# Optimization experiments

Measured on AMD Instinct MI355X. Metric: run time of the kernel, lower is better.

The kernel has to match this reference:

```python
import math
import jax, jax.numpy as jnp
import numpy as np

CT = {"SDD": 1000.0, "SCD": 500.0, "det_interval": 1.0, "num_det": 736}


def ramp_filter_np(ct, scale):
    # Standard equiangular fan-beam ramp filter (utility.ramp_filter):
    #   h[0] = 1/(8*db^2); h[n odd] = -1/(2*(pi*sin(n*db))^2); h[n even!=0] = 0
    db = ct["det_interval"] / ct["SDD"] * scale  # angular detector pitch at this scale
    n_det = int(ct["num_det"] // scale)
    n = np.arange(-(n_det - 1), n_det)  # length K = 2*n_det - 1
    h = np.zeros(n.shape, dtype=np.float32)
    h[n == 0] = 1.0 / (8.0 * db ** 2)
    odd = (n % 2) != 0
    h[odd] = -0.5 / (np.pi * np.sin(n[odd] * db)) ** 2
    return h


def setup_inputs() -> dict:
    key = jax.random.key(0)
    scale = 1
    batch, ch, view, det = 16, 1, 1152, CT["num_det"] // scale
    sinogram = jax.random.normal(key, (batch, ch, view, det), dtype=jnp.float32)
    delta_b = CT["det_interval"] / CT["SDD"]
    # recon_filter = ramp_filter * scale * delta_b, shaped [1,1,1,K] (OIHW)
    filt = ramp_filter_np(CT, scale) * scale * delta_b
    recon_filter = jnp.asarray(filt, dtype=jnp.float32)[None, None, None, :]
    return {"sinogram": sinogram, "recon_filter": recon_filter, "scale": scale}


def reference(sinogram, recon_filter, scale):
    det = sinogram.shape[-1]
    # cosine fan-beam pre-weighting
    s_range = (CT["det_interval"]
               * jnp.linspace((1.0 - det) / 2.0, (det - 1.0) / 2.0, det, dtype=jnp.float32)
               * scale) / CT["SDD"]
    cos_weight = (CT["SCD"] / 10000.0) * jnp.cos(s_range)  # [det]
    x = sinogram * cos_weight[None, None, None, :]
    # 1D ramp-filter convolution along detector axis (F.conv2d with 1xK kernel)
    K = recon_filter.shape[-1]
    pad = K // 2
    out = jax.lax.conv_general_dilated(
        x, recon_filter,
        window_strides=(1, 1),
        padding=[(0, 0), (pad, pad)],
        dimension_numbers=("NCHW", "OIHW", "NCHW"),
    )
    return out
```

## Files before the change

### kernel.cpp

```cpp
#include <hip/hip_runtime.h>

typedef unsigned short ushort_t;
typedef ushort_t u16x8 __attribute__((ext_vector_type(8)));
typedef __bf16 bf16x8 __attribute__((ext_vector_type(8)));
typedef float f32x4 __attribute__((ext_vector_type(4)));

#define DET 736
#define NPAD 768
#define NKB 23
#define NBY 12

__device__ __forceinline__ ushort_t f2bf(float f) {
    unsigned u = __builtin_bit_cast(unsigned, f);
    u += 0x7FFFu + ((u >> 16) & 1u);
    return (ushort_t)(u >> 16);
}

__global__ void cast_swz_a(const float* __restrict__ in, ushort_t* __restrict__ out) {
    int t = blockIdx.x * 256 + threadIdx.x;
    int l  = t & 63;
    int fi = t >> 6;
    int kb = fi % NKB;
    int rs = fi / NKB;
    int row = rs * 16 + (l & 15);
    int k0  = kb * 32 + (l >> 4) * 8;
    const float* p = in + row * DET + k0;
    float4 a = *(const float4*)p;
    float4 b = *(const float4*)(p + 4);
    u16x8 o;
    o[0] = f2bf(a.x); o[1] = f2bf(a.y); o[2] = f2bf(a.z); o[3] = f2bf(a.w);
    o[4] = f2bf(b.x); o[5] = f2bf(b.y); o[6] = f2bf(b.z); o[7] = f2bf(b.w);
    *(u16x8*)(out + (size_t)t * 8) = o;
}

__global__ void prep_bt_swz(const float* __restrict__ filt, ushort_t* __restrict__ B) {
    int G = blockIdx.x * 256 + threadIdx.x;
    int l  = G & 63;
    int ns = (G >> 6) & 3;
    int kb = (G >> 8) % NKB;
    int by = (G >> 8) / NKB;
    int col = by * 64 + ns * 16 + (l & 15);
    int k0  = kb * 32 + (l >> 4) * 8;
    u16x8 o;
#pragma unroll
    for (int j = 0; j < 8; ++j) {
        int k = k0 + j;
        float w = 0.05f * cosf(((float)k - 367.5f) * 0.001f);
        float v = (col < DET) ? w * filt[k - col + (DET - 1)] : 0.0f;
        o[j] = f2bf(v);
    }
    *(u16x8*)(B + (size_t)G * 8) = o;
}

__global__ __launch_bounds__(256, 3) void gemm_nb(
    const ushort_t* __restrict__ A,
    const ushort_t* __restrict__ B,
    float* __restrict__ C)
{
    __shared__ ushort_t Bs[12 * 256 * 8];

    const int tid  = threadIdx.x;
    const int lane = tid & 63;
    const int w    = tid >> 6;
    const int quad = lane >> 4;
    const int l16  = lane & 15;
    const int bx = blockIdx.x, by = blockIdx.y;

    const ushort_t* pA = A + ((size_t)(bx * 16 + w * 4) * NKB * 64 + lane) * 8;
    const ushort_t* pB = B + (size_t)by * (NKB * 256) * 8;

    f32x4 acc[4][4];
#pragma unroll
    for (int i = 0; i < 4; ++i)
#pragma unroll
        for (int j = 0; j < 4; ++j)
            acc[i][j] = (f32x4){0.f, 0.f, 0.f, 0.f};

#define STAGE(CHUNKS, OFF)                                            \
    for (int c = tid; c < (CHUNKS); c += 256)                         \
        *(u16x8*)(Bs + (size_t)c * 8) = *(const u16x8*)(pB + ((size_t)(OFF) + c) * 8);

#define BODY(KB, KB0)                                                          \
    {                                                                          \
        u16x8 af[4], bf[4];                                                    \
        _Pragma("unroll")                                                      \
        for (int mi = 0; mi < 4; ++mi)                                         \
            af[mi] = *(const u16x8*)(pA + ((size_t)mi * NKB * 64 + (KB) * 64) * 8); \
        _Pragma("unroll")                                                      \
        for (int ni = 0; ni < 4; ++ni)                                         \
            bf[ni] = *(const u16x8*)(Bs + (((KB) - (KB0)) * 256 + ni * 64 + lane) * 8); \
        _Pragma("unroll")                                                      \
        for (int mi = 0; mi < 4; ++mi)                                         \
            _Pragma("unroll")                                                  \
            for (int ni = 0; ni < 4; ++ni)                                     \
                acc[mi][ni] = __builtin_amdgcn_mfma_f32_16x16x32_bf16(         \
                    __builtin_bit_cast(bf16x8, af[mi]),                        \
                    __builtin_bit_cast(bf16x8, bf[ni]),                        \
                    acc[mi][ni], 0, 0, 0);                                     \
    }

    STAGE(12 * 256, 0)
    __syncthreads();
#pragma unroll
    for (int kb = 0; kb < 12; ++kb) BODY(kb, 0)
    __syncthreads();
    STAGE(11 * 256, 12 * 256)
    __syncthreads();
#pragma unroll
    for (int kb = 12; kb < 23; ++kb) BODY(kb, 12)

#pragma unroll
    for (int mi = 0; mi < 4; ++mi) {
#pragma unroll
        for (int ni = 0; ni < 4; ++ni) {
            int colg = by * 64 + ni * 16 + l16;
            if (colg < DET) {
#pragma unroll
                for (int r = 0; r < 4; ++r) {
                    size_t rowg = (size_t)bx * 256 + w * 64 + mi * 16 + quad * 4 + r;
                    C[rowg * DET + colg] = acc[mi][ni][r];
                }
            }
        }
    }
#undef STAGE
#undef BODY
}

extern "C" void kernel_launch(void* const* d_in, const int* in_sizes, int n_in,
                              void* d_out, int out_size, void* d_ws, size_t ws_size,
                              hipStream_t stream) {
    const float* sino = (const float*)d_in[0];
    const float* filt = (const float*)d_in[1];
    int total = in_sizes[0];

    ushort_t* Aswz = (ushort_t*)d_ws;
    ushort_t* Bswz = Aswz + (size_t)total;
    float* out = (float*)d_out;

    cast_swz_a<<<total / 8 / 256, 256, 0, stream>>>(sino, Aswz);
    prep_bt_swz<<<(NBY * NKB * 4 * 64) / 256, 256, 0, stream>>>(filt, Bswz);

    dim3 grid(18432 / 256, NBY);
    gemm_nb<<<grid, 256, 0, stream>>>(Aswz, Bswz, out);
}
```

Before: 144.0 us.

## Fuse fp32-to-bf16 cast of sinogram into GEMM, stage A in LDS

Removes the separate cast/swizzle kernel and its bf16 workspace round-trip. Each GEMM block now loads 32 rows of fp32 sinogram, converts them to bf16 into shared memory, and computes all 736 output columns. Each wave covers three column panels and reads the filter matrix B directly from global memory (L2) rather than staging it in LDS. This saves a kernel launch and the A write/read traffic, but every block re-reads the whole B matrix, the grid becomes a single 1D dimension of 576 blocks, and each block does less A reuse per B load.

```diff
diff --git a/kernel.cpp b/kernel.cpp
--- a/kernel.cpp
+++ b/kernel.cpp
@@ -6,31 +6,13 @@
 typedef float f32x4 __attribute__((ext_vector_type(4)));
 
 #define DET 736
-#define NPAD 768
 #define NKB 23
-#define NBY 12
+#define NPAN 12
 
 __device__ __forceinline__ ushort_t f2bf(float f) {
     unsigned u = __builtin_bit_cast(unsigned, f);
     u += 0x7FFFu + ((u >> 16) & 1u);
     return (ushort_t)(u >> 16);
-}
-
-__global__ void cast_swz_a(const float* __restrict__ in, ushort_t* __restrict__ out) {
-    int t = blockIdx.x * 256 + threadIdx.x;
-    int l  = t & 63;
-    int fi = t >> 6;
-    int kb = fi % NKB;
-    int rs = fi / NKB;
-    int row = rs * 16 + (l & 15);
-    int k0  = kb * 32 + (l >> 4) * 8;
-    const float* p = in + row * DET + k0;
-    float4 a = *(const float4*)p;
-    float4 b = *(const float4*)(p + 4);
-    u16x8 o;
-    o[0] = f2bf(a.x); o[1] = f2bf(a.y); o[2] = f2bf(a.z); o[3] = f2bf(a.w);
-    o[4] = f2bf(b.x); o[5] = f2bf(b.y); o[6] = f2bf(b.z); o[7] = f2bf(b.w);
-    *(u16x8*)(out + (size_t)t * 8) = o;
 }
 
 __global__ void prep_bt_swz(const float* __restrict__ filt, ushort_t* __restrict__ B) {
@@ -52,79 +34,83 @@
     *(u16x8*)(B + (size_t)G * 8) = o;
 }
 
-__global__ __launch_bounds__(256, 3) void gemm_nb(
-    const ushort_t* __restrict__ A,
+__global__ __launch_bounds__(256, 3) void gemm_f(
+    const float* __restrict__ A,
     const ushort_t* __restrict__ B,
     float* __restrict__ C)
 {
-    __shared__ ushort_t Bs[12 * 256 * 8];
+    __shared__ ushort_t As[2944 * 8];
 
     const int tid  = threadIdx.x;
     const int lane = tid & 63;
     const int w    = tid >> 6;
     const int quad = lane >> 4;
     const int l16  = lane & 15;
-    const int bx = blockIdx.x, by = blockIdx.y;
+    const size_t r0 = (size_t)blockIdx.x * 32;
 
-    const ushort_t* pA = A + ((size_t)(bx * 16 + w * 4) * NKB * 64 + lane) * 8;
-    const ushort_t* pB = B + (size_t)by * (NKB * 256) * 8;
+    for (int c = tid; c < 2944; c += 256) {
+        int l  = c & 63;
+        int t  = c >> 6;
+        int kb = t % NKB;
+        int rs = t / NKB;
+        int row = rs * 16 + (l & 15);
+        int k0  = kb * 32 + (l >> 4) * 8;
+        const float* p = A + (r0 + row) * DET + k0;
+        float4 x = *(const float4*)p;
+        float4 y = *(const float4*)(p + 4);
+        u16x8 o;
+        o[0] = f2bf(x.x); o[1] = f2bf(x.y); o[2] = f2bf(x.z); o[3] = f2bf(x.w);
+        o[4] = f2bf(y.x); o[5] = f2bf(y.y); o[6] = f2bf(y.z); o[7] = f2bf(y.w);
+        *(u16x8*)(As + (size_t)c * 8) = o;
+    }
+    __syncthreads();
 
-    f32x4 acc[4][4];
+    f32x4 acc[3][2][4];
 #pragma unroll
-    for (int i = 0; i < 4; ++i)
+    for (int cg = 0; cg < 3; ++cg)
 #pragma unroll
-        for (int j = 0; j < 4; ++j)
-            acc[i][j] = (f32x4){0.f, 0.f, 0.f, 0.f};
+        for (int mi = 0; mi < 2; ++mi)
+#pragma unroll
+            for (int ni = 0; ni < 4; ++ni)
+                acc[cg][mi][ni] = (f32x4){0.f, 0.f, 0.f, 0.f};
 
-#define STAGE(CHUNKS, OFF)                                            \
-    for (int c = tid; c < (CHUNKS); c += 256)                         \
-        *(u16x8*)(Bs + (size_t)c * 8) = *(const u16x8*)(pB + ((size_t)(OFF) + c) * 8);
-
-#define BODY(KB, KB0)                                                          \
-    {                                                                          \
-        u16x8 af[4], bf[4];                                                    \
-        _Pragma("unroll")                                                      \
-        for (int mi = 0; mi < 4; ++mi)                                         \
-            af[mi] = *(const u16x8*)(pA + ((size_t)mi * NKB * 64 + (KB) * 64) * 8); \
-        _Pragma("unroll")                                                      \
-        for (int ni = 0; ni < 4; ++ni)                                         \
-            bf[ni] = *(const u16x8*)(Bs + (((KB) - (KB0)) * 256 + ni * 64 + lane) * 8); \
-        _Pragma("unroll")                                                      \
-        for (int mi = 0; mi < 4; ++mi)                                         \
-            _Pragma("unroll")                                                  \
-            for (int ni = 0; ni < 4; ++ni)                                     \
-                acc[mi][ni] = __builtin_amdgcn_mfma_f32_16x16x32_bf16(         \
-                    __builtin_bit_cast(bf16x8, af[mi]),                        \
-                    __builtin_bit_cast(bf16x8, bf[ni]),                        \
-                    acc[mi][ni], 0, 0, 0);                                     \
-    }
-
-    STAGE(12 * 256, 0)
-    __syncthreads();
+    for (int kb = 0; kb < NKB; ++kb) {
+        u16x8 af[2];
 #pragma unroll
-    for (int kb = 0; kb < 12; ++kb) BODY(kb, 0)
-    __syncthreads();
-    STAGE(11 * 256, 12 * 256)
-    __syncthreads();
+        for (int mi = 0; mi < 2; ++mi)
+            af[mi] = *(const u16x8*)(As + ((size_t)(mi * NKB + kb) * 64 + lane) * 8);
 #pragma unroll
-    for (int kb = 12; kb < 23; ++kb) BODY(kb, 12)
-
+        for (int cg = 0; cg < 3; ++cg) {
+            const ushort_t* pB = B + ((size_t)((cg * 4 + w) * NKB + kb) * 4 * 64 + lane) * 8;
 #pragma unroll
-    for (int mi = 0; mi < 4; ++mi) {
+            for (int ni = 0; ni < 4; ++ni) {
+                u16x8 bfv = *(const u16x8*)(pB + (size_t)ni * 64 * 8);
 #pragma unroll
-        for (int ni = 0; ni < 4; ++ni) {
-            int colg = by * 64 + ni * 16 + l16;
-            if (colg < DET) {
-#pragma unroll
-                for (int r = 0; r < 4; ++r) {
-                    size_t rowg = (size_t)bx * 256 + w * 64 + mi * 16 + quad * 4 + r;
-                    C[rowg * DET + colg] = acc[mi][ni][r];
-                }
+                for (int mi = 0; mi < 2; ++mi)
+                    acc[cg][mi][ni] = __builtin_amdgcn_mfma_f32_16x16x32_bf16(
+                        __builtin_bit_cast(bf16x8, af[mi]),
+                        __builtin_bit_cast(bf16x8, bfv),
+                        acc[cg][mi][ni], 0, 0, 0);
             }
         }
     }
-#undef STAGE
-#undef BODY
+
+#pragma unroll
+    for (int cg = 0; cg < 3; ++cg) {
+#pragma unroll
+        for (int ni = 0; ni < 4; ++ni) {
+            int colg = (cg * 4 + w) * 64 + ni * 16 + l16;
+            if (colg < DET) {
+#pragma unroll
+                for (int mi = 0; mi < 2; ++mi)
+#pragma unroll
+                    for (int r = 0; r < 4; ++r) {
+                        size_t rowg = r0 + mi * 16 + quad * 4 + r;
+                        C[rowg * DET + colg] = acc[cg][mi][ni][r];
+                    }
+            }
+        }
+    }
 }
 
 extern "C" void kernel_launch(void* const* d_in, const int* in_sizes, int n_in,
@@ -133,14 +119,12 @@
     const float* sino = (const float*)d_in[0];
     const float* filt = (const float*)d_in[1];
     int total = in_sizes[0];
+    int M = total / DET;
 
-    ushort_t* Aswz = (ushort_t*)d_ws;
-    ushort_t* Bswz = Aswz + (size_t)total;
+    ushort_t* Bswz = (ushort_t*)d_ws;
     float* out = (float*)d_out;
 
-    cast_swz_a<<<total / 8 / 256, 256, 0, stream>>>(sino, Aswz);
-    prep_bt_swz<<<(NBY * NKB * 4 * 64) / 256, 256, 0, stream>>>(filt, Bswz);
+    prep_bt_swz<<<(NPAN * NKB * 4 * 64) / 256, 256, 0, stream>>>(filt, Bswz);
 
-    dim3 grid(18432 / 256, NBY);
-    gemm_nb<<<grid, 256, 0, stream>>>(Aswz, Bswz, out);
+    gemm_f<<<M / 32, 256, 0, stream>>>(sino, Bswz, out);
 }
```

After: 142.4 us. No clear change (-1.1%).
